# Kernel optimization log

Hardware: AMD Instinct MI355X
Metric: run time of the kernel (lower is better)

Reference implementation:

```python
import jax, jax.numpy as jnp
import numpy as np

# dims matching init_kwargs / input_specs
N, C, H, W = 8, 256, 64, 64
OUT_C, KH, KW = 256, 3, 3
STRIDE, PAD = 1, 1
OUT_H = (H - KH + 2 * PAD) // STRIDE + 1  # 64
OUT_W = (W - KW + 2 * PAD) // STRIDE + 1  # 64
K = KH * KW


def setup_inputs() -> dict:
    key = jax.random.key(0)
    k1, k2, k3 = jax.random.split(key, 3)
    x = jax.random.normal(k1, (N, C, H, W), dtype=jnp.float32)
    offset = jax.random.normal(k2, (N, 2 * K, OUT_H, OUT_W), dtype=jnp.float32)
    # kaiming-uniform-ish scale for weight (fan_in = C*KH*KW)
    bound = 1.0 / np.sqrt(C * KH * KW)
    weight = jax.random.uniform(k3, (OUT_C, C, KH, KW), dtype=jnp.float32,
                                minval=-bound, maxval=bound)
    return {"input": x, "offset": offset, "weight": weight}


def _deform_conv(x, offset, weight):
    # base sampling positions in pixel coords: y = oy*stride + ky - pad
    ky = jnp.repeat(jnp.arange(KH, dtype=jnp.float32) - PAD, KW)  # [K]
    kx = jnp.tile(jnp.arange(KW, dtype=jnp.float32) - PAD, KH)    # [K]
    oy = jnp.arange(OUT_H, dtype=jnp.float32) * STRIDE            # [outH]
    ox = jnp.arange(OUT_W, dtype=jnp.float32) * STRIDE            # [outW]
    base_y = ky[:, None, None] + oy[None, :, None]  # [K, outH, 1]
    base_x = kx[:, None, None] + ox[None, None, :]  # [K, 1, outW]

    off = offset.reshape(N, K, 2, OUT_H, OUT_W)
    y = base_y[None] + off[:, :, 0]  # [N, K, outH, outW], offset channel 0 = dy
    xp = base_x[None] + off[:, :, 1]  # channel 1 = dx

    # bilinear sample with zero padding (grid_sample align_corners=True, zeros)
    y0 = jnp.floor(y)
    x0 = jnp.floor(xp)
    bidx = jnp.arange(N)[:, None, None, None]
    acc = jnp.zeros((N, K, OUT_H, OUT_W, C), dtype=x.dtype)
    for dy in (0.0, 1.0):
        for dx in (0.0, 1.0):
            yi = y0 + dy
            xi = x0 + dx
            wgt = (1.0 - jnp.abs(y - yi)) * (1.0 - jnp.abs(xp - xi))
            valid = ((yi >= 0) & (yi <= H - 1) & (xi >= 0) & (xi <= W - 1))
            yc = jnp.clip(yi, 0, H - 1).astype(jnp.int32)
            xc = jnp.clip(xi, 0, W - 1).astype(jnp.int32)
            g = x[bidx, :, yc, xc]  # [N, K, outH, outW, C]
            acc = acc + g * (wgt * valid.astype(x.dtype))[..., None]

    # weight.view(outC, -1) flattens (C, KH, KW) -> (C, K) ordering
    w = weight.reshape(OUT_C, C, K)
    out = jnp.einsum('nkhwc,ock->nohw', acc, w)  # [N, outC, outH, outW]
    return out


def reference(input, offset, weight):
    # NOTE: original forward never adds bias -> faithfully omitted
    return _deform_conv(input, offset, weight)
```

## Files before the change

### kernel.cpp

```cpp
#include <hip/hip_runtime.h>
#include <hip/hip_bf16.h>
#include <hip/hip_fp16.h>
#include <stdint.h>


typedef short short8 __attribute__((ext_vector_type(8)));
typedef float f32x4 __attribute__((ext_vector_type(4)));

__device__ __forceinline__ float bflo(uint32_t u) { return __uint_as_float(u << 16); }
__device__ __forceinline__ float bfhi(uint32_t u) { return __uint_as_float(u & 0xffff0000u); }
__device__ __forceinline__ uint32_t packbf(float a, float b) {
  unsigned short ua = __builtin_bit_cast(unsigned short, __float2bfloat16(a));
  unsigned short ub = __builtin_bit_cast(unsigned short, __float2bfloat16(b));
  return (uint32_t)ua | ((uint32_t)ub << 16);
}
__device__ __forceinline__ float h2f(uint32_t bits16) {
  __half h = __builtin_bit_cast(__half, (unsigned short)bits16);
  return __half2float(h);
}

__global__ __launch_bounds__(256) void prep_x_kernel(const float* __restrict__ x,
                                                     unsigned short* __restrict__ xb) {
  __shared__ float tile[64][65];
  int bn   = blockIdx.x >> 8;
  int rem  = blockIdx.x & 255;
  int y    = rem >> 2;
  int cblk = rem & 3;
  int tid  = threadIdx.x;
  const float* src = x + ((size_t)(bn * 256 + cblk * 64)) * 4096 + y * 64;
#pragma unroll
  for (int i = 0; i < 4; ++i) {
    int u  = i * 256 + tid;
    int cl = u >> 4;
    int xs = (u & 15) * 4;
    float4 v = *(const float4*)(src + cl * 4096 + xs);
    tile[cl][xs] = v.x; tile[cl][xs + 1] = v.y;
    tile[cl][xs + 2] = v.z; tile[cl][xs + 3] = v.w;
  }
  __syncthreads();
  unsigned short* dst = xb + ((size_t)(bn * 64 + y) * 64) * 256 + cblk * 64;
#pragma unroll
  for (int i = 0; i < 8; ++i) {
    int v2  = i * 256 + tid;
    int xc  = v2 >> 5;
    int cl2 = (v2 & 31) * 2;
    *(uint32_t*)(dst + xc * 256 + cl2) = packbf(tile[cl2][xc], tile[cl2 + 1][xc]);
  }
}

__global__ __launch_bounds__(256) void prep_wc_kernel(const float* __restrict__ w,
                                                      const float* __restrict__ offset,
                                                      unsigned short* __restrict__ w3s,
                                                      unsigned short* __restrict__ coords) {
  if (blockIdx.x < 2304) {
    int idx = blockIdx.x * 256 + threadIdx.x;
    int t   = idx >> 14;
    int r2  = idx & 16383;
    int g   = r2 >> 3;
    int e   = r2 & 7;
    int oc  = g >> 3;
    int kk8 = (g & 7) ^ (oc & 7);
    int kk  = kk8 * 8 + e;
    int c   = (t & 3) * 64 + kk;
    int k   = t >> 2;
    w3s[idx] = __builtin_bit_cast(unsigned short, __float2bfloat16(w[(oc * 256 + c) * 9 + k]));
  } else {
    int idx = (blockIdx.x - 2304) * 256 + threadIdx.x;
    int ow  = idx & 63;
    int oh  = (idx >> 6) & 63;
    int r   = idx >> 12;
    int k   = r % 9;
    int bn  = r / 9;
    int ky = k / 3 - 1;
    int kx = k % 3 - 1;
    float offy = offset[((bn * 18 + 2 * k    ) * 64 + oh) * 64 + ow];
    float offx = offset[((bn * 18 + 2 * k + 1) * 64 + oh) * 64 + ow];
    float y = (float)(oh + ky) + offy;
    float x = (float)(ow + kx) + offx;
    float y0f = floorf(y), x0f = floorf(x);
    float fy = y - y0f, fx = x - x0f;
    int y0 = (int)y0f, x0 = (int)x0f;
    int y1 = y0 + 1, x1 = x0 + 1;
    float vy0 = (y0 >= 0 && y0 <= 63) ? 1.0f : 0.0f;
    float vy1 = (y1 >= 0 && y1 <= 63) ? 1.0f : 0.0f;
    float vx0 = (x0 >= 0 && x0 <= 63) ? 1.0f : 0.0f;
    float vx1 = (x1 >= 0 && x1 <= 63) ? 1.0f : 0.0f;
    float wy0 = (1.0f - fy) * vy0, wy1 = fy * vy1;
    float wx0 = (1.0f - fx) * vx0, wx1 = fx * vx1;
    int y0c = min(max(y0, 0), 63), y1c = min(max(y1, 0), 63);
    int x0c = min(max(x0, 0), 63), x1c = min(max(x1, 0), 63);
    unsigned short ent[8];
    ent[0] = __builtin_bit_cast(unsigned short, __float2half(wy0 * wx0));
    ent[1] = __builtin_bit_cast(unsigned short, __float2half(wy0 * wx1));
    ent[2] = __builtin_bit_cast(unsigned short, __float2half(wy1 * wx0));
    ent[3] = __builtin_bit_cast(unsigned short, __float2half(wy1 * wx1));
    ent[4] = (unsigned short)(y0c * 64 + x0c);
    ent[5] = (unsigned short)(y0c * 64 + x1c);
    ent[6] = (unsigned short)(y1c * 64 + x0c);
    ent[7] = (unsigned short)(y1c * 64 + x1c);
    *(uint4*)(coords + (size_t)idx * 8) = *(const uint4*)ent;
  }
}

__global__ __launch_bounds__(512, 4) void deform_mfma_kernel(
    const unsigned short* __restrict__ xb,
    const unsigned short* __restrict__ coords,
    const unsigned short* __restrict__ w3s,
    float* __restrict__ out) {
  __shared__ __align__(16) unsigned short At[64 * 72];
  __shared__ __align__(16) unsigned short Bt[256 * 64];

  int bn  = blockIdx.x & 7;
  int oh  = blockIdx.x >> 3;
  int tid = threadIdx.x;

  int w     = tid >> 6;
  int lane  = tid & 63;
  int wrow  = w & 1;
  int wcol  = w >> 1;
  int mrow  = lane & 15;
  int quad  = lane >> 4;

  int srow = tid >> 3;
  int sg   = tid & 7;

  const unsigned short* xbn = xb + (size_t)bn * (64 * 64 * 256);
  const char* gbase = (const char*)xbn + sg * 16;
  const unsigned short* cbase = coords + ((size_t)((bn * 9) * 64 + oh) * 64 + srow) * 8;

  f32x4 acc[2][4] = {};

#define BDMA(TT)                                                                \
  {                                                                             \
    const unsigned short* src = w3s + (TT) * 16384;                             \
    _Pragma("unroll")                                                           \
    for (int j = 0; j < 4; ++j) {                                               \
      int base16 = j * 512 + w * 64;                                            \
      __builtin_amdgcn_global_load_lds(                                         \
          (const __attribute__((address_space(1))) void*)(src + (base16 + lane) * 8), \
          (__attribute__((address_space(3))) void*)(Bt + base16 * 8),           \
          16, 0, 0);                                                            \
    }                                                                           \
  }

#define ASTAGE(TT)                                                              \
  {                                                                             \
    uint4 e = *(const uint4*)(cbase + ((TT) >> 2) * 32768);                     \
    const char* gb = gbase + ((TT) & 3) * 128;                                  \
    uint4 c00 = *(const uint4*)(gb + ((e.z & 0xffffu) << 9));                   \
    uint4 c01 = *(const uint4*)(gb + ((e.z >> 16) << 9));                       \
    uint4 c10 = *(const uint4*)(gb + ((e.w & 0xffffu) << 9));                   \
    uint4 c11 = *(const uint4*)(gb + ((e.w >> 16) << 9));                       \
    float w00 = h2f(e.x & 0xffffu), w01 = h2f(e.x >> 16);                       \
    float w10 = h2f(e.y & 0xffffu), w11 = h2f(e.y >> 16);                       \
    float a0 = bflo(c00.x) * w00 + bflo(c01.x) * w01 + bflo(c10.x) * w10 + bflo(c11.x) * w11; \
    float a1 = bfhi(c00.x) * w00 + bfhi(c01.x) * w01 + bfhi(c10.x) * w10 + bfhi(c11.x) * w11; \
    float a2 = bflo(c00.y) * w00 + bflo(c01.y) * w01 + bflo(c10.y) * w10 + bflo(c11.y) * w11; \
    float a3 = bfhi(c00.y) * w00 + bfhi(c01.y) * w01 + bfhi(c10.y) * w10 + bfhi(c11.y) * w11; \
    float a4 = bflo(c00.z) * w00 + bflo(c01.z) * w01 + bflo(c10.z) * w10 + bflo(c11.z) * w11; \
    float a5 = bfhi(c00.z) * w00 + bfhi(c01.z) * w01 + bfhi(c10.z) * w10 + bfhi(c11.z) * w11; \
    float a6 = bflo(c00.w) * w00 + bflo(c01.w) * w01 + bflo(c10.w) * w10 + bflo(c11.w) * w11; \
    float a7 = bfhi(c00.w) * w00 + bfhi(c01.w) * w01 + bfhi(c10.w) * w10 + bfhi(c11.w) * w11; \
    uint4 pk;                                                                   \
    pk.x = packbf(a0, a1); pk.y = packbf(a2, a3);                               \
    pk.z = packbf(a4, a5); pk.w = packbf(a6, a7);                               \
    *(uint4*)(&At[srow * 72 + sg * 8]) = pk;                                    \
  }

  BDMA(0)
  ASTAGE(0)
  __syncthreads();

  short8 af[2][2];
  short8 bfr[2][4];

  for (int t = 0; t < 36; ++t) {
#pragma unroll
    for (int ks = 0; ks < 2; ++ks) {
#pragma unroll
      for (int m = 0; m < 2; ++m)
        af[m][ks] = *(const short8*)(&At[(wrow * 32 + m * 16 + mrow) * 72 + ks * 32 + quad * 8]);
#pragma unroll
      for (int nn = 0; nn < 4; ++nn) {
        int oc  = wcol * 64 + nn * 16 + mrow;
        int g16 = oc * 8 + ((ks * 4 + quad) ^ (mrow & 7));
        bfr[ks][nn] = *(const short8*)(Bt + g16 * 8);
      }
    }
    __syncthreads();

    if (t < 35) {
      BDMA(t + 1)
      ASTAGE(t + 1)
    }
#pragma unroll
    for (int ks = 0; ks < 2; ++ks)
#pragma unroll
      for (int m = 0; m < 2; ++m)
#pragma unroll
        for (int nn = 0; nn < 4; ++nn)
          acc[m][nn] = __builtin_amdgcn_mfma_f32_16x16x32_bf16(af[m][ks], bfr[ks][nn], acc[m][nn], 0, 0, 0);
    __syncthreads();
  }

  float* outp = out + (size_t)(bn * 256) * 4096 + oh * 64;
#pragma unroll
  for (int m = 0; m < 2; ++m) {
    int ow0 = wrow * 32 + m * 16 + quad * 4;
#pragma unroll
    for (int nn = 0; nn < 4; ++nn) {
      int oc = wcol * 64 + nn * 16 + mrow;
      *(f32x4*)(outp + oc * 4096 + ow0) = acc[m][nn];
    }
  }
#undef BDMA
#undef ASTAGE
}

extern "C" void kernel_launch(void* const* d_in, const int* in_sizes, int n_in,
                              void* d_out, int out_size, void* d_ws, size_t ws_size,
                              hipStream_t stream) {
  (void)in_sizes; (void)n_in; (void)out_size; (void)ws_size;
  const float* x      = (const float*)d_in[0];
  const float* offset = (const float*)d_in[1];
  const float* weight = (const float*)d_in[2];
  float* out = (float*)d_out;

  unsigned short* xb     = (unsigned short*)d_ws;
  unsigned short* w3s    = xb + (size_t)8 * 64 * 64 * 256;
  unsigned short* coords = w3s + (size_t)36 * 16384;

  prep_x_kernel<<<2048, 256, 0, stream>>>(x, xb);
  prep_wc_kernel<<<3456, 256, 0, stream>>>(weight, offset, w3s, coords);
  deform_mfma_kernel<<<512, 512, 0, stream>>>(xb, coords, w3s, out);
}
```

Baseline: 155.3 us.

## Merge prep kernels and prefetch bilinear gathers one stage ahead

Folds the two preprocessing kernels into a single launch that dispatches by block index, removing one kernel launch and its boundary. In the main MFMA loop, the four gathered corner loads for the next-next tile are issued a step earlier and held in registers, with interpolation done at write time. The coordinate entry is also loaded ahead so gather latency can overlap the MFMA work. This adds register pressure from the extra live uint4 values.

```diff
diff --git a/kernel.cpp b/kernel.cpp
--- a/kernel.cpp
+++ b/kernel.cpp
@@ -19,41 +19,40 @@
   return __half2float(h);
 }
 
-__global__ __launch_bounds__(256) void prep_x_kernel(const float* __restrict__ x,
-                                                     unsigned short* __restrict__ xb) {
+__global__ __launch_bounds__(256) void prep_all_kernel(const float* __restrict__ x,
+                                                       const float* __restrict__ w,
+                                                       const float* __restrict__ offset,
+                                                       unsigned short* __restrict__ xb,
+                                                       unsigned short* __restrict__ w3s,
+                                                       unsigned short* __restrict__ coords) {
   __shared__ float tile[64][65];
-  int bn   = blockIdx.x >> 8;
-  int rem  = blockIdx.x & 255;
-  int y    = rem >> 2;
-  int cblk = rem & 3;
-  int tid  = threadIdx.x;
-  const float* src = x + ((size_t)(bn * 256 + cblk * 64)) * 4096 + y * 64;
-#pragma unroll
-  for (int i = 0; i < 4; ++i) {
-    int u  = i * 256 + tid;
-    int cl = u >> 4;
-    int xs = (u & 15) * 4;
-    float4 v = *(const float4*)(src + cl * 4096 + xs);
-    tile[cl][xs] = v.x; tile[cl][xs + 1] = v.y;
-    tile[cl][xs + 2] = v.z; tile[cl][xs + 3] = v.w;
-  }
-  __syncthreads();
-  unsigned short* dst = xb + ((size_t)(bn * 64 + y) * 64) * 256 + cblk * 64;
-#pragma unroll
-  for (int i = 0; i < 8; ++i) {
-    int v2  = i * 256 + tid;
-    int xc  = v2 >> 5;
-    int cl2 = (v2 & 31) * 2;
-    *(uint32_t*)(dst + xc * 256 + cl2) = packbf(tile[cl2][xc], tile[cl2 + 1][xc]);
-  }
-}
-
-__global__ __launch_bounds__(256) void prep_wc_kernel(const float* __restrict__ w,
-                                                      const float* __restrict__ offset,
-                                                      unsigned short* __restrict__ w3s,
-                                                      unsigned short* __restrict__ coords) {
-  if (blockIdx.x < 2304) {
-    int idx = blockIdx.x * 256 + threadIdx.x;
+  int tid = threadIdx.x;
+  if (blockIdx.x < 2048) {
+    int bn   = blockIdx.x >> 8;
+    int rem  = blockIdx.x & 255;
+    int y    = rem >> 2;
+    int cblk = rem & 3;
+    const float* src = x + ((size_t)(bn * 256 + cblk * 64)) * 4096 + y * 64;
+#pragma unroll
+    for (int i = 0; i < 4; ++i) {
+      int u  = i * 256 + tid;
+      int cl = u >> 4;
+      int xs = (u & 15) * 4;
+      float4 v = *(const float4*)(src + cl * 4096 + xs);
+      tile[cl][xs] = v.x; tile[cl][xs + 1] = v.y;
+      tile[cl][xs + 2] = v.z; tile[cl][xs + 3] = v.w;
+    }
+    __syncthreads();
+    unsigned short* dst = xb + ((size_t)(bn * 64 + y) * 64) * 256 + cblk * 64;
+#pragma unroll
+    for (int i = 0; i < 8; ++i) {
+      int v2  = i * 256 + tid;
+      int xc  = v2 >> 5;
+      int cl2 = (v2 & 31) * 2;
+      *(uint32_t*)(dst + xc * 256 + cl2) = packbf(tile[cl2][xc], tile[cl2 + 1][xc]);
+    }
+  } else if (blockIdx.x < 4352) {
+    int idx = (blockIdx.x - 2048) * 256 + tid;
     int t   = idx >> 14;
     int r2  = idx & 16383;
     int g   = r2 >> 3;
@@ -65,7 +64,7 @@
     int k   = t >> 2;
     w3s[idx] = __builtin_bit_cast(unsigned short, __float2bfloat16(w[(oc * 256 + c) * 9 + k]));
   } else {
-    int idx = (blockIdx.x - 2304) * 256 + threadIdx.x;
+    int idx = (blockIdx.x - 4352) * 256 + tid;
     int ow  = idx & 63;
     int oh  = (idx >> 6) & 63;
     int r   = idx >> 12;
@@ -76,9 +75,9 @@
     float offy = offset[((bn * 18 + 2 * k    ) * 64 + oh) * 64 + ow];
     float offx = offset[((bn * 18 + 2 * k + 1) * 64 + oh) * 64 + ow];
     float y = (float)(oh + ky) + offy;
-    float x = (float)(ow + kx) + offx;
-    float y0f = floorf(y), x0f = floorf(x);
-    float fy = y - y0f, fx = x - x0f;
+    float x2 = (float)(ow + kx) + offx;
+    float y0f = floorf(y), x0f = floorf(x2);
+    float fy = y - y0f, fx = x2 - x0f;
     int y0 = (int)y0f, x0 = (int)x0f;
     int y1 = y0 + 1, x1 = x0 + 1;
     float vy0 = (y0 >= 0 && y0 <= 63) ? 1.0f : 0.0f;
@@ -143,32 +142,44 @@
     }                                                                           \
   }
 
-#define ASTAGE(TT)                                                              \
+#define CLOAD(D00, D01, D10, D11, EV, CH)                                       \
   {                                                                             \
-    uint4 e = *(const uint4*)(cbase + ((TT) >> 2) * 32768);                     \
-    const char* gb = gbase + ((TT) & 3) * 128;                                  \
-    uint4 c00 = *(const uint4*)(gb + ((e.z & 0xffffu) << 9));                   \
-    uint4 c01 = *(const uint4*)(gb + ((e.z >> 16) << 9));                       \
-    uint4 c10 = *(const uint4*)(gb + ((e.w & 0xffffu) << 9));                   \
-    uint4 c11 = *(const uint4*)(gb + ((e.w >> 16) << 9));                       \
-    float w00 = h2f(e.x & 0xffffu), w01 = h2f(e.x >> 16);                       \
-    float w10 = h2f(e.y & 0xffffu), w11 = h2f(e.y >> 16);                       \
-    float a0 = bflo(c00.x) * w00 + bflo(c01.x) * w01 + bflo(c10.x) * w10 + bflo(c11.x) * w11; \
-    float a1 = bfhi(c00.x) * w00 + bfhi(c01.x) * w01 + bfhi(c10.x) * w10 + bfhi(c11.x) * w11; \
-    float a2 = bflo(c00.y) * w00 + bflo(c01.y) * w01 + bflo(c10.y) * w10 + bflo(c11.y) * w11; \
-    float a3 = bfhi(c00.y) * w00 + bfhi(c01.y) * w01 + bfhi(c10.y) * w10 + bfhi(c11.y) * w11; \
-    float a4 = bflo(c00.z) * w00 + bflo(c01.z) * w01 + bflo(c10.z) * w10 + bflo(c11.z) * w11; \
-    float a5 = bfhi(c00.z) * w00 + bfhi(c01.z) * w01 + bfhi(c10.z) * w10 + bfhi(c11.z) * w11; \
-    float a6 = bflo(c00.w) * w00 + bflo(c01.w) * w01 + bflo(c10.w) * w10 + bflo(c11.w) * w11; \
-    float a7 = bfhi(c00.w) * w00 + bfhi(c01.w) * w01 + bfhi(c10.w) * w10 + bfhi(c11.w) * w11; \
+    const char* gb_ = gbase + (CH) * 128;                                       \
+    D00 = *(const uint4*)(gb_ + (((EV).z & 0xffffu) << 9));                     \
+    D01 = *(const uint4*)(gb_ + (((EV).z >> 16) << 9));                         \
+    D10 = *(const uint4*)(gb_ + (((EV).w & 0xffffu) << 9));                     \
+    D11 = *(const uint4*)(gb_ + (((EV).w >> 16) << 9));                         \
+  }
+
+#define INTERP_WRITE(C00, C01, C10, C11, WX, WY)                                \
+  {                                                                             \
+    float w00 = h2f((WX) & 0xffffu), w01 = h2f((WX) >> 16);                     \
+    float w10 = h2f((WY) & 0xffffu), w11 = h2f((WY) >> 16);                     \
+    float a0 = bflo(C00.x) * w00 + bflo(C01.x) * w01 + bflo(C10.x) * w10 + bflo(C11.x) * w11; \
+    float a1 = bfhi(C00.x) * w00 + bfhi(C01.x) * w01 + bfhi(C10.x) * w10 + bfhi(C11.x) * w11; \
+    float a2 = bflo(C00.y) * w00 + bflo(C01.y) * w01 + bflo(C10.y) * w10 + bflo(C11.y) * w11; \
+    float a3 = bfhi(C00.y) * w00 + bfhi(C01.y) * w01 + bfhi(C10.y) * w10 + bfhi(C11.y) * w11; \
+    float a4 = bflo(C00.z) * w00 + bflo(C01.z) * w01 + bflo(C10.z) * w10 + bflo(C11.z) * w11; \
+    float a5 = bfhi(C00.z) * w00 + bfhi(C01.z) * w01 + bfhi(C10.z) * w10 + bfhi(C11.z) * w11; \
+    float a6 = bflo(C00.w) * w00 + bflo(C01.w) * w01 + bflo(C10.w) * w10 + bflo(C11.w) * w11; \
+    float a7 = bfhi(C00.w) * w00 + bfhi(C01.w) * w01 + bfhi(C10.w) * w10 + bfhi(C11.w) * w11; \
     uint4 pk;                                                                   \
     pk.x = packbf(a0, a1); pk.y = packbf(a2, a3);                               \
     pk.z = packbf(a4, a5); pk.w = packbf(a6, a7);                               \
     *(uint4*)(&At[srow * 72 + sg * 8]) = pk;                                    \
   }
 
+  uint4 eR = *(const uint4*)(cbase);
+  {
+    uint4 p00, p01, p10, p11;
+    CLOAD(p00, p01, p10, p11, eR, 0)
+    INTERP_WRITE(p00, p01, p10, p11, eR.x, eR.y)
+  }
   BDMA(0)
-  ASTAGE(0)
+  uint4 c00, c01, c10, c11;
+  uint32_t wx, wy;
+  CLOAD(c00, c01, c10, c11, eR, 1)
+  wx = eR.x; wy = eR.y;
   __syncthreads();
 
   short8 af[2][2];
@@ -191,8 +202,15 @@
 
     if (t < 35) {
       BDMA(t + 1)
-      ASTAGE(t + 1)
-    }
+      INTERP_WRITE(c00, c01, c10, c11, wx, wy)
+    }
+    if (t <= 33) {
+      CLOAD(c00, c01, c10, c11, eR, ((t + 2) & 3))
+      wx = eR.x; wy = eR.y;
+    }
+    if ((t & 3) == 1 && t <= 29)
+      eR = *(const uint4*)(cbase + ((t + 6) >> 2) * 32768);
+
 #pragma unroll
     for (int ks = 0; ks < 2; ++ks)
 #pragma unroll
@@ -214,7 +232,8 @@
     }
   }
 #undef BDMA
-#undef ASTAGE
+#undef CLOAD
+#undef INTERP_WRITE
 }
 
 extern "C" void kernel_launch(void* const* d_in, const int* in_sizes, int n_in,
@@ -230,7 +249,6 @@
   unsigned short* w3s    = xb + (size_t)8 * 64 * 64 * 256;
   unsigned short* coords = w3s + (size_t)36 * 16384;
 
-  prep_x_kernel<<<2048, 256, 0, stream>>>(x, xb);
-  prep_wc_kernel<<<3456, 256, 0, stream>>>(weight, offset, w3s, coords);
+  prep_all_kernel<<<5504, 256, 0, stream>>>(x, weight, offset, xb, w3s, coords);
   deform_mfma_kernel<<<512, 512, 0, stream>>>(xb, coords, w3s, out);
 }
```

After: 161.8 us. 1.04x slower.
